# Performance work log

Measured on AMD Instinct MI355X. Metric: run time of the kernel, lower is better.

## Reference

```python
import jax, jax.numpy as jnp
import numpy as np

N, E, DIN, DH, DOUT = 50000, 800000, 256, 128, 64


def setup_inputs() -> dict:
    key = jax.random.key(0)
    ks = jax.random.split(key, 12)
    return {
        "h": jax.random.normal(ks[0], (N, DIN), jnp.float32),
        "src": jax.random.randint(ks[1], (E,), 0, N, jnp.int32),
        "dst": jax.random.randint(ks[2], (E,), 0, N, jnp.int32),
        "W1": jax.random.normal(ks[3], (DIN, DH), jnp.float32) * (DIN ** -0.5),
        "al1": jax.random.normal(ks[4], (DH,), jnp.float32) * (DH ** -0.5),
        "ar1": jax.random.normal(ks[5], (DH,), jnp.float32) * (DH ** -0.5),
        "W2": jax.random.normal(ks[6], (DH, DH), jnp.float32) * (DH ** -0.5),
        "al2": jax.random.normal(ks[7], (DH,), jnp.float32) * (DH ** -0.5),
        "ar2": jax.random.normal(ks[8], (DH,), jnp.float32) * (DH ** -0.5),
        "W3": jax.random.normal(ks[9], (DH, DOUT), jnp.float32) * (DH ** -0.5),
        "al3": jax.random.normal(ks[10], (DOUT,), jnp.float32) * (DOUT ** -0.5),
        "ar3": jax.random.normal(ks[11], (DOUT,), jnp.float32) * (DOUT ** -0.5),
    }


def gat_layer(h, W, al, ar, src, dst):
    """DGL GATConv, 1 head, no bias: proj -> leaky_relu edge scores -> edge softmax over dst -> scatter-sum."""
    n = h.shape[0]
    f = h @ W                                   # [N, d]
    el = f @ al                                 # [N]
    er = f @ ar                                 # [N]
    e = jax.nn.leaky_relu(el[src] + er[dst], negative_slope=0.2)  # [E]
    m = jax.ops.segment_max(e, dst, num_segments=n)
    m = jnp.where(jnp.isfinite(m), m, 0.0)      # zero-in-degree nodes
    m = jax.lax.stop_gradient(m)
    ex = jnp.exp(e - m[dst])                    # [E]
    z = jax.ops.segment_sum(ex, dst, num_segments=n)
    a = ex / jnp.maximum(z, 1e-9)[dst]          # [E] softmax weights
    return jax.ops.segment_sum(a[:, None] * f[src], dst, num_segments=n)


def reference(h, src, dst, W1, al1, ar1, W2, al2, ar2, W3, al3, ar3):
    x = gat_layer(h, W1, al1, ar1, src, dst)
    x = jax.nn.relu(x)                          # dropout = identity (eval)
    x = gat_layer(x, W2, al2, ar2, src, dst)
    x = jax.nn.relu(x)
    x = gat_layer(x, W3, al3, ar3, src, dst)    # mean over 1 head = identity
    return jax.nn.log_softmax(x, axis=-1)
```

## Files before the change

kernel.cpp:

```cpp
#include <hip/hip_runtime.h>
#include <math.h>

#define DIN 256
#define DHID 128
#define DOUTC 64
#define EPB 2048

typedef __attribute__((ext_vector_type(8))) short short8;
typedef __attribute__((ext_vector_type(4))) float f32x4;

static __device__ __forceinline__ float wave_max(float v){
  #pragma unroll
  for (int o=1;o<64;o<<=1) v = fmaxf(v, __shfl_xor(v,o,64));
  return v;
}
static __device__ __forceinline__ float wave_sum(float v){
  #pragma unroll
  for (int o=1;o<64;o<<=1) v += __shfl_xor(v,o,64);
  return v;
}

static __device__ __forceinline__ unsigned short bf16_rne(float x){
  unsigned int u = __float_as_uint(x);
  return (unsigned short)((u + 0x7FFFu + ((u>>16)&1u)) >> 16);
}
static __device__ __forceinline__ float bf16_to_f32(unsigned short h){
  return __uint_as_float(((unsigned int)h)<<16);
}
static __device__ __forceinline__ float blo(unsigned int u){ return __uint_as_float(u<<16); }
static __device__ __forceinline__ float bhi(unsigned int u){ return __uint_as_float(u & 0xffff0000u); }

__global__ __launch_bounds__(256) void rs_hist(const int* __restrict__ dst,
    int* __restrict__ ghist, int E, int NB){
  __shared__ int h[256];
  const int t = threadIdx.x, blk = blockIdx.x;
  h[t] = 0; __syncthreads();
  const int base = blk*EPB;
  #pragma unroll
  for (int i=0;i<EPB/256;i++){
    int j = base + i*256 + t;
    if (j < E) atomicAdd(&h[dst[j]>>8], 1);
  }
  __syncthreads();
  ghist[t*NB + blk] = h[t];
}

__global__ __launch_bounds__(256) void rs_scan(int* __restrict__ ghist,
    int* __restrict__ btot, int NB){
  __shared__ int b[256];
  __shared__ int carry;
  const int hb = blockIdx.x, t = threadIdx.x;
  if (t==0) carry = 0;
  __syncthreads();
  for (int c0=0; c0<NB; c0+=256){
    int i = c0 + t;
    int v = (i<NB)? ghist[hb*NB+i] : 0;
    b[t] = v; __syncthreads();
    #pragma unroll
    for (int o=1;o<256;o<<=1){
      int x = (t>=o)? b[t-o] : 0;
      __syncthreads();
      b[t] += x;
      __syncthreads();
    }
    if (i<NB) ghist[hb*NB+i] = carry + b[t] - v;
    __syncthreads();
    if (t==255) carry += b[255];
    __syncthreads();
  }
  if (t==255) btot[hb] = carry;
}

__global__ __launch_bounds__(256) void rs_scan2(int* __restrict__ btot,
    int* __restrict__ offsets, int N, int E){
  __shared__ int b[256];
  const int t = threadIdx.x;
  int v = btot[t];
  b[t] = v; __syncthreads();
  #pragma unroll
  for (int o=1;o<256;o<<=1){
    int x = (t>=o)? b[t-o] : 0;
    __syncthreads();
    b[t] += x;
    __syncthreads();
  }
  btot[t] = b[t] - v;
  if (t==255){ btot[256] = E; offsets[N] = E; }
}

__global__ __launch_bounds__(256) void rs_scatter(const int* __restrict__ src,
    const int* __restrict__ dst, const int* __restrict__ ghist,
    const int* __restrict__ btot, unsigned int* __restrict__ ebuf, int E, int NB){
  __shared__ int cur[256];
  const int t = threadIdx.x, blk = blockIdx.x;
  cur[t] = ghist[t*NB + blk] + btot[t];
  __syncthreads();
  const int base = blk*EPB;
  #pragma unroll
  for (int i=0;i<EPB/256;i++){
    int j = base + i*256 + t;
    if (j < E){
      int d = dst[j];
      int pos = atomicAdd(&cur[d>>8], 1);
      ebuf[pos] = ((unsigned)src[j] << 8) | ((unsigned)d & 255u);
    }
  }
}

__global__ __launch_bounds__(256) void bucket_sort(const unsigned int* __restrict__ ebuf,
    const int* __restrict__ btot, int* __restrict__ offsets,
    int* __restrict__ srcs, int N){
  __shared__ int h[256];
  __shared__ int b[256];
  const int hb = blockIdx.x, t = threadIdx.x;
  const int b0 = btot[hb], b1 = btot[hb+1];
  h[t] = 0; __syncthreads();
  for (int j=b0+t; j<b1; j+=256) atomicAdd(&h[ebuf[j] & 255u], 1);
  __syncthreads();
  int v = h[t];
  b[t] = v; __syncthreads();
  #pragma unroll
  for (int o=1;o<256;o<<=1){
    int x = (t>=o)? b[t-o] : 0;
    __syncthreads();
    b[t] += x;
    __syncthreads();
  }
  const int excl = b[t] - v;
  const int node = hb*256 + t;
  if (node < N) offsets[node] = b0 + excl;
  h[t] = excl;
  __syncthreads();
  for (int j=b0+t; j<b1; j+=256){
    unsigned int e = ebuf[j];
    int pos = b0 + atomicAdd(&h[e & 255u], 1);
    srcs[pos] = (int)(e >> 8);
  }
}

template<int K, int NC>
static __device__ __forceinline__ void pack_one(const float* __restrict__ W,
    unsigned short* __restrict__ Wp, int idx){
  constexpr int CT = NC/16;
  int l = idx & 63, t = idx >> 6;
  int ct = t % CT, kt = t / CT;
  int col = ct*16 + (l & 15);
  int k0 = kt*32 + (l >> 4)*8;
  unsigned short* dstp = Wp + (size_t)idx*8;
  #pragma unroll
  for (int j=0;j<8;j++)
    dstp[j] = bf16_rne(W[(size_t)(k0+j)*NC + col]);
}

__global__ __launch_bounds__(256) void pack_all(const float* __restrict__ W1,
    const float* __restrict__ W2, const float* __restrict__ W3,
    unsigned short* __restrict__ Wp1, unsigned short* __restrict__ Wp2,
    unsigned short* __restrict__ Wp3){
  constexpr int N1 = (DIN/32)*(DHID/16)*64;
  constexpr int N2 = (DHID/32)*(DHID/16)*64;
  constexpr int N3 = (DHID/32)*(DOUTC/16)*64;
  int idx = blockIdx.x*256 + threadIdx.x;
  if (idx < N1) pack_one<DIN,DHID>(W1, Wp1, idx);
  else if (idx < N1+N2) pack_one<DHID,DHID>(W2, Wp2, idx-N1);
  else if (idx < N1+N2+N3) pack_one<DHID,DOUTC>(W3, Wp3, idx-N1-N2);
}

template<int K, int NC>
__global__ __launch_bounds__(256) void gemm_v3(const float* __restrict__ A,
    const unsigned short* __restrict__ Wp,
    const float* __restrict__ al, const float* __restrict__ ar,
    unsigned short* __restrict__ Fb, float* __restrict__ el, float* __restrict__ er, int nrows)
{
  constexpr int CT = NC/16, KT = K/32;
  constexpr int CHUNK_KT = (32/CT) < KT ? (32/CT) : KT;
  constexpr int NCHUNK = KT / CHUNK_KT;
  constexpr int CHUNK_SHORTS = CHUNK_KT*CT*64*8;
  __shared__ unsigned short bsm[CHUNK_SHORTS];

  const int tid = threadIdx.x;
  const int lane = tid & 63;
  const int wid  = tid >> 6;
  const int row0 = blockIdx.x*64 + wid*16;
  const int c = lane & 15, g = lane >> 4;
  const int arow = row0 + c;
  const bool aok = arow < nrows;

  f32x4 acc[CT];
  #pragma unroll
  for (int i=0;i<CT;i++) acc[i] = (f32x4)0.f;

  for (int ch=0; ch<NCHUNK; ++ch){
    if (ch) __syncthreads();
    {
      const uint4* gsrc = (const uint4*)Wp + (size_t)ch*(CHUNK_SHORTS/8);
      uint4* ldst = (uint4*)bsm;
      #pragma unroll
      for (int i=0; i<CHUNK_SHORTS/8/256; ++i)
        ldst[i*256 + tid] = gsrc[i*256 + tid];
    }
    __syncthreads();

    #pragma unroll
    for (int ktl=0; ktl<CHUNK_KT; ++ktl){
      const int k0 = (ch*CHUNK_KT + ktl)*32 + g*8;
      float xs[8];
      if (aok){
        float4 v0 = *(const float4*)&A[(size_t)arow*K + k0];
        float4 v1 = *(const float4*)&A[(size_t)arow*K + k0 + 4];
        xs[0]=v0.x; xs[1]=v0.y; xs[2]=v0.z; xs[3]=v0.w;
        xs[4]=v1.x; xs[5]=v1.y; xs[6]=v1.z; xs[7]=v1.w;
      } else {
        #pragma unroll
        for (int j=0;j<8;j++) xs[j]=0.f;
      }
      short8 ahi, alo;
      #pragma unroll
      for (int j=0;j<8;j++){
        unsigned short hh = bf16_rne(xs[j]);
        ahi[j] = (short)hh;
        alo[j] = (short)bf16_rne(xs[j] - bf16_to_f32(hh));
      }
      #pragma unroll
      for (int ct=0; ct<CT; ++ct){
        short8 b = *(const short8*)&bsm[(ktl*CT+ct)*512 + lane*8];
        acc[ct] = __builtin_amdgcn_mfma_f32_16x16x32_bf16(ahi, b, acc[ct], 0,0,0);
        acc[ct] = __builtin_amdgcn_mfma_f32_16x16x32_bf16(alo, b, acc[ct], 0,0,0);
      }
    }
  }

  float alv[CT], arv[CT];
  #pragma unroll
  for (int ct=0;ct<CT;ct++){ alv[ct]=al[ct*16+c]; arv[ct]=ar[ct*16+c]; }
  #pragma unroll
  for (int j=0;j<4;j++){
    const int row = row0 + g*4 + j;
    const bool ok = row < nrows;
    float sl=0.f, sr=0.f;
    #pragma unroll
    for (int ct=0;ct<CT;ct++){
      float f = acc[ct][j];
      sl = fmaf(f, alv[ct], sl);
      sr = fmaf(f, arv[ct], sr);
      if (ok) Fb[(size_t)row*NC + ct*16 + c] = bf16_rne(f);
    }
    #pragma unroll
    for (int o=1;o<16;o<<=1){ sl += __shfl_xor(sl,o,64); sr += __shfl_xor(sr,o,64); }
    if (ok && c==0){ el[row]=sl; er[row]=sr; }
  }
}

template<int D, bool RELU, bool LOGSM>
__global__ __launch_bounds__(256) void agg7_kernel(const unsigned short* __restrict__ Fb,
    const float* __restrict__ el, const float* __restrict__ er,
    const int* __restrict__ offsets, const int* __restrict__ srcs,
    float* __restrict__ out, int N)
{
  constexpr int CPL = D/16;
  __shared__ float2 ws[4][64];
  const int wv = threadIdx.x >> 6;
  const int lane = threadIdx.x & 63;
  const int c16 = lane & 15, g = lane >> 4;
  const int v = blockIdx.x*4 + wv;
  if (v >= N) return;
  const int o0 = offsets[v], o1 = offsets[v+1];
  const float erv = er[v];

  float zlane = 0.f;
  float acc[CPL];
  #pragma unroll
  for (int i=0;i<CPL;i++) acc[i]=0.f;

  for (int s0 = o0; s0 < o1; s0 += 64){
    const int j = s0 + lane;
    int sidx = 0; float wgt = 0.f;
    if (j < o1){
      sidx = srcs[j];
      float tv = el[sidx] + erv;
      tv = (tv > 0.f) ? tv : 0.2f*tv;
      wgt = __expf(tv);
    }
    zlane += wgt;
    ws[wv][lane] = make_float2(wgt, __int_as_float(sidx));
    __builtin_amdgcn_wave_barrier();

    const int cnt = min(64, o1 - s0);
    int t = g;
    if constexpr (D == 128){
      for (; t+4 < cnt; t += 8){
        float2 p0 = ws[wv][t], p1 = ws[wv][t+4];
        uint4 u0 = *((const uint4*)(Fb + (size_t)__float_as_int(p0.y)*128) + c16);
        uint4 u1 = *((const uint4*)(Fb + (size_t)__float_as_int(p1.y)*128) + c16);
        acc[0]=fmaf(p0.x, blo(u0.x), acc[0]); acc[1]=fmaf(p0.x, bhi(u0.x), acc[1]);
        acc[2]=fmaf(p0.x, blo(u0.y), acc[2]); acc[3]=fmaf(p0.x, bhi(u0.y), acc[3]);
        acc[4]=fmaf(p0.x, blo(u0.z), acc[4]); acc[5]=fmaf(p0.x, bhi(u0.z), acc[5]);
        acc[6]=fmaf(p0.x, blo(u0.w), acc[6]); acc[7]=fmaf(p0.x, bhi(u0.w), acc[7]);
        acc[0]=fmaf(p1.x, blo(u1.x), acc[0]); acc[1]=fmaf(p1.x, bhi(u1.x), acc[1]);
        acc[2]=fmaf(p1.x, blo(u1.y), acc[2]); acc[3]=fmaf(p1.x, bhi(u1.y), acc[3]);
        acc[4]=fmaf(p1.x, blo(u1.z), acc[4]); acc[5]=fmaf(p1.x, bhi(u1.z), acc[5]);
        acc[6]=fmaf(p1.x, blo(u1.w), acc[6]); acc[7]=fmaf(p1.x, bhi(u1.w), acc[7]);
      }
      if (t < cnt){
        float2 p0 = ws[wv][t];
        uint4 u0 = *((const uint4*)(Fb + (size_t)__float_as_int(p0.y)*128) + c16);
        acc[0]=fmaf(p0.x, blo(u0.x), acc[0]); acc[1]=fmaf(p0.x, bhi(u0.x), acc[1]);
        acc[2]=fmaf(p0.x, blo(u0.y), acc[2]); acc[3]=fmaf(p0.x, bhi(u0.y), acc[3]);
        acc[4]=fmaf(p0.x, blo(u0.z), acc[4]); acc[5]=fmaf(p0.x, bhi(u0.z), acc[5]);
        acc[6]=fmaf(p0.x, blo(u0.w), acc[6]); acc[7]=fmaf(p0.x, bhi(u0.w), acc[7]);
      }
    } else {
      for (; t+4 < cnt; t += 8){
        float2 p0 = ws[wv][t], p1 = ws[wv][t+4];
        uint2 u0 = *((const uint2*)(Fb + (size_t)__float_as_int(p0.y)*64) + c16);
        uint2 u1 = *((const uint2*)(Fb + (size_t)__float_as_int(p1.y)*64) + c16);
        acc[0]=fmaf(p0.x, blo(u0.x), acc[0]); acc[1]=fmaf(p0.x, bhi(u0.x), acc[1]);
        acc[2]=fmaf(p0.x, blo(u0.y), acc[2]); acc[3]=fmaf(p0.x, bhi(u0.y), acc[3]);
        acc[0]=fmaf(p1.x, blo(u1.x), acc[0]); acc[1]=fmaf(p1.x, bhi(u1.x), acc[1]);
        acc[2]=fmaf(p1.x, blo(u1.y), acc[2]); acc[3]=fmaf(p1.x, bhi(u1.y), acc[3]);
      }
      if (t < cnt){
        float2 p0 = ws[wv][t];
        uint2 u0 = *((const uint2*)(Fb + (size_t)__float_as_int(p0.y)*64) + c16);
        acc[0]=fmaf(p0.x, blo(u0.x), acc[0]); acc[1]=fmaf(p0.x, bhi(u0.x), acc[1]);
        acc[2]=fmaf(p0.x, blo(u0.y), acc[2]); acc[3]=fmaf(p0.x, bhi(u0.y), acc[3]);
      }
    }
    __builtin_amdgcn_wave_barrier();
  }

  #pragma unroll
  for (int i=0;i<CPL;i++){
    acc[i] += __shfl_xor(acc[i],16,64);
    acc[i] += __shfl_xor(acc[i],32,64);
  }
  const float z = wave_sum(zlane);
  const float zi = 1.f / fmaxf(z, 1e-9f);

  if constexpr (LOGSM){
    float y[CPL];
    #pragma unroll
    for (int i=0;i<CPL;i++) y[i] = acc[i]*zi;
    float M = y[0];
    #pragma unroll
    for (int i=1;i<CPL;i++) M = fmaxf(M, y[i]);
    #pragma unroll
    for (int o=1;o<16;o<<=1) M = fmaxf(M, __shfl_xor(M,o,64));
    float ssum = 0.f;
    #pragma unroll
    for (int i=0;i<CPL;i++) ssum += __expf(y[i]-M);
    #pragma unroll
    for (int o=1;o<16;o<<=1) ssum += __shfl_xor(ssum,o,64);
    const float lw = M + logf(ssum);
    if (g==0){
      float4 r = make_float4(y[0]-lw, y[1]-lw, y[2]-lw, y[3]-lw);
      *(float4*)&out[(size_t)v*64 + c16*4] = r;
    }
  } else {
    if (g==0){
      float r[CPL];
      #pragma unroll
      for (int i=0;i<CPL;i++){ r[i]=acc[i]*zi; if (RELU) r[i]=fmaxf(r[i],0.f); }
      *(float4*)&out[(size_t)v*128 + c16*8]     = make_float4(r[0],r[1],r[2],r[3]);
      *(float4*)&out[(size_t)v*128 + c16*8 + 4] = make_float4(r[4],r[5],r[6],r[7]);
    }
  }
}

extern "C" void kernel_launch(void* const* d_in, const int* in_sizes, int n_in,
                              void* d_out, int out_size, void* d_ws, size_t ws_size,
                              hipStream_t stream) {
  const float* h   = (const float*)d_in[0];
  const int*   src = (const int*)d_in[1];
  const int*   dst = (const int*)d_in[2];
  const float* W1  = (const float*)d_in[3];
  const float* al1 = (const float*)d_in[4];
  const float* ar1 = (const float*)d_in[5];
  const float* W2  = (const float*)d_in[6];
  const float* al2 = (const float*)d_in[7];
  const float* ar2 = (const float*)d_in[8];
  const float* W3  = (const float*)d_in[9];
  const float* al3 = (const float*)d_in[10];
  const float* ar3 = (const float*)d_in[11];

  const int N = in_sizes[0] / DIN;
  const int E = in_sizes[1];
  const int NB = (E + EPB - 1) / EPB;
  const int NHB = (N + 255) / 256;

  auto alignup = [](size_t x){ return (x + 255) & ~(size_t)255; };
  char* p = (char*)d_ws;
  int* offsets = (int*)p; p += alignup(((size_t)N+1)*4);
  int* srcs    = (int*)p; p += alignup((size_t)E*4);
  int* ghist   = (int*)p; p += alignup((size_t)256*NB*4);
  int* btot    = (int*)p; p += alignup(257*4);
  unsigned int* ebuf = (unsigned int*)p; p += alignup((size_t)E*4);
  unsigned short* Fb = (unsigned short*)p; p += alignup((size_t)N*DHID*2);
  float* X     = (float*)p; p += alignup((size_t)N*DHID*4);
  float* el    = (float*)p; p += alignup((size_t)N*4);
  float* er    = (float*)p; p += alignup((size_t)N*4);
  unsigned short* Wp1 = (unsigned short*)p; p += alignup((size_t)(DIN/32)*(DHID/16)*64*8*2);
  unsigned short* Wp2 = (unsigned short*)p; p += alignup((size_t)(DHID/32)*(DHID/16)*64*8*2);
  unsigned short* Wp3 = (unsigned short*)p; p += alignup((size_t)(DHID/32)*(DOUTC/16)*64*8*2);

  const int nbW4 = (N+3)/4;
  const int nbG  = (N+63)/64;

  pack_all<<<28,256,0,stream>>>(W1, W2, W3, Wp1, Wp2, Wp3);

  rs_hist   <<<NB, 256,0,stream>>>(dst, ghist, E, NB);
  rs_scan   <<<256,256,0,stream>>>(ghist, btot, NB);
  rs_scan2  <<<1,  256,0,stream>>>(btot, offsets, N, E);
  rs_scatter<<<NB, 256,0,stream>>>(src, dst, ghist, btot, ebuf, E, NB);
  bucket_sort<<<NHB,256,0,stream>>>(ebuf, btot, offsets, srcs, N);

  gemm_v3<DIN,DHID><<<nbG,256,0,stream>>>(h, Wp1, al1, ar1, Fb, el, er, N);
  agg7_kernel<128,true,false><<<nbW4,256,0,stream>>>(Fb, el, er, offsets, srcs, X, N);

  gemm_v3<DHID,DHID><<<nbG,256,0,stream>>>(X, Wp2, al2, ar2, Fb, el, er, N);
  agg7_kernel<128,true,false><<<nbW4,256,0,stream>>>(Fb, el, er, offsets, srcs, X, N);

  gemm_v3<DHID,DOUTC><<<nbG,256,0,stream>>>(X, Wp3, al3, ar3, Fb, el, er, N);
  agg7_kernel<64,false,true><<<nbW4,256,0,stream>>>(Fb, el, er, offsets, srcs, (float*)d_out, N);
}
```

Measured before the change: 169.7 us.

## Fuse CSR build and weight packing into one cooperative kernel with grid syncs

Merges the six preprocessing kernels (weight pack, histogram, two scans, scatter, bucket sort) into a single cooperative launch, using grid-wide syncs between phases. Weight packing runs alongside the histogram on extra blocks. The aim is to remove per-launch gaps and tail effects for these small kernels. In exchange, grid syncs add their own cost, and the grid (about 391+28 blocks) must fit co-resident or the launch fails.

```diff
diff --git a/kernel.cpp b/kernel.cpp
--- a/kernel.cpp
+++ b/kernel.cpp
@@ -1,4 +1,5 @@
 #include <hip/hip_runtime.h>
+#include <hip/hip_cooperative_groups.h>
 #include <math.h>
 
 #define DIN 256
@@ -9,11 +10,6 @@
 typedef __attribute__((ext_vector_type(8))) short short8;
 typedef __attribute__((ext_vector_type(4))) float f32x4;
 
-static __device__ __forceinline__ float wave_max(float v){
-  #pragma unroll
-  for (int o=1;o<64;o<<=1) v = fmaxf(v, __shfl_xor(v,o,64));
-  return v;
-}
 static __device__ __forceinline__ float wave_sum(float v){
   #pragma unroll
   for (int o=1;o<64;o<<=1) v += __shfl_xor(v,o,64);
@@ -29,114 +25,6 @@
 }
 static __device__ __forceinline__ float blo(unsigned int u){ return __uint_as_float(u<<16); }
 static __device__ __forceinline__ float bhi(unsigned int u){ return __uint_as_float(u & 0xffff0000u); }
-
-__global__ __launch_bounds__(256) void rs_hist(const int* __restrict__ dst,
-    int* __restrict__ ghist, int E, int NB){
-  __shared__ int h[256];
-  const int t = threadIdx.x, blk = blockIdx.x;
-  h[t] = 0; __syncthreads();
-  const int base = blk*EPB;
-  #pragma unroll
-  for (int i=0;i<EPB/256;i++){
-    int j = base + i*256 + t;
-    if (j < E) atomicAdd(&h[dst[j]>>8], 1);
-  }
-  __syncthreads();
-  ghist[t*NB + blk] = h[t];
-}
-
-__global__ __launch_bounds__(256) void rs_scan(int* __restrict__ ghist,
-    int* __restrict__ btot, int NB){
-  __shared__ int b[256];
-  __shared__ int carry;
-  const int hb = blockIdx.x, t = threadIdx.x;
-  if (t==0) carry = 0;
-  __syncthreads();
-  for (int c0=0; c0<NB; c0+=256){
-    int i = c0 + t;
-    int v = (i<NB)? ghist[hb*NB+i] : 0;
-    b[t] = v; __syncthreads();
-    #pragma unroll
-    for (int o=1;o<256;o<<=1){
-      int x = (t>=o)? b[t-o] : 0;
-      __syncthreads();
-      b[t] += x;
-      __syncthreads();
-    }
-    if (i<NB) ghist[hb*NB+i] = carry + b[t] - v;
-    __syncthreads();
-    if (t==255) carry += b[255];
-    __syncthreads();
-  }
-  if (t==255) btot[hb] = carry;
-}
-
-__global__ __launch_bounds__(256) void rs_scan2(int* __restrict__ btot,
-    int* __restrict__ offsets, int N, int E){
-  __shared__ int b[256];
-  const int t = threadIdx.x;
-  int v = btot[t];
-  b[t] = v; __syncthreads();
-  #pragma unroll
-  for (int o=1;o<256;o<<=1){
-    int x = (t>=o)? b[t-o] : 0;
-    __syncthreads();
-    b[t] += x;
-    __syncthreads();
-  }
-  btot[t] = b[t] - v;
-  if (t==255){ btot[256] = E; offsets[N] = E; }
-}
-
-__global__ __launch_bounds__(256) void rs_scatter(const int* __restrict__ src,
-    const int* __restrict__ dst, const int* __restrict__ ghist,
-    const int* __restrict__ btot, unsigned int* __restrict__ ebuf, int E, int NB){
-  __shared__ int cur[256];
-  const int t = threadIdx.x, blk = blockIdx.x;
-  cur[t] = ghist[t*NB + blk] + btot[t];
-  __syncthreads();
-  const int base = blk*EPB;
-  #pragma unroll
-  for (int i=0;i<EPB/256;i++){
-    int j = base + i*256 + t;
-    if (j < E){
-      int d = dst[j];
-      int pos = atomicAdd(&cur[d>>8], 1);
-      ebuf[pos] = ((unsigned)src[j] << 8) | ((unsigned)d & 255u);
-    }
-  }
-}
-
-__global__ __launch_bounds__(256) void bucket_sort(const unsigned int* __restrict__ ebuf,
-    const int* __restrict__ btot, int* __restrict__ offsets,
-    int* __restrict__ srcs, int N){
-  __shared__ int h[256];
-  __shared__ int b[256];
-  const int hb = blockIdx.x, t = threadIdx.x;
-  const int b0 = btot[hb], b1 = btot[hb+1];
-  h[t] = 0; __syncthreads();
-  for (int j=b0+t; j<b1; j+=256) atomicAdd(&h[ebuf[j] & 255u], 1);
-  __syncthreads();
-  int v = h[t];
-  b[t] = v; __syncthreads();
-  #pragma unroll
-  for (int o=1;o<256;o<<=1){
-    int x = (t>=o)? b[t-o] : 0;
-    __syncthreads();
-    b[t] += x;
-    __syncthreads();
-  }
-  const int excl = b[t] - v;
-  const int node = hb*256 + t;
-  if (node < N) offsets[node] = b0 + excl;
-  h[t] = excl;
-  __syncthreads();
-  for (int j=b0+t; j<b1; j+=256){
-    unsigned int e = ebuf[j];
-    int pos = b0 + atomicAdd(&h[e & 255u], 1);
-    srcs[pos] = (int)(e >> 8);
-  }
-}
 
 template<int K, int NC>
 static __device__ __forceinline__ void pack_one(const float* __restrict__ W,
@@ -152,17 +40,118 @@
     dstp[j] = bf16_rne(W[(size_t)(k0+j)*NC + col]);
 }
 
-__global__ __launch_bounds__(256) void pack_all(const float* __restrict__ W1,
-    const float* __restrict__ W2, const float* __restrict__ W3,
-    unsigned short* __restrict__ Wp1, unsigned short* __restrict__ Wp2,
-    unsigned short* __restrict__ Wp3){
-  constexpr int N1 = (DIN/32)*(DHID/16)*64;
-  constexpr int N2 = (DHID/32)*(DHID/16)*64;
-  constexpr int N3 = (DHID/32)*(DOUTC/16)*64;
-  int idx = blockIdx.x*256 + threadIdx.x;
-  if (idx < N1) pack_one<DIN,DHID>(W1, Wp1, idx);
-  else if (idx < N1+N2) pack_one<DHID,DHID>(W2, Wp2, idx-N1);
-  else if (idx < N1+N2+N3) pack_one<DHID,DOUTC>(W3, Wp3, idx-N1-N2);
+__global__ __launch_bounds__(256) void csr_coop(
+    const int* __restrict__ src, const int* __restrict__ dst,
+    const float* __restrict__ W1, const float* __restrict__ W2, const float* __restrict__ W3,
+    unsigned short* __restrict__ Wp1, unsigned short* __restrict__ Wp2, unsigned short* __restrict__ Wp3,
+    int* __restrict__ ghist, int* __restrict__ btot, int* __restrict__ offsets,
+    unsigned int* __restrict__ ebuf, int* __restrict__ srcs,
+    int E, int N, int NB, int NHB)
+{
+  cooperative_groups::grid_group gg = cooperative_groups::this_grid();
+  __shared__ int h[256];
+  __shared__ int b[256];
+  const int t = threadIdx.x, blk = blockIdx.x;
+
+  if (blk < NB){
+    h[t] = 0; __syncthreads();
+    const int base = blk*EPB;
+    #pragma unroll
+    for (int i=0;i<EPB/256;i++){
+      int j = base + i*256 + t;
+      if (j < E) atomicAdd(&h[dst[j]>>8], 1);
+    }
+    __syncthreads();
+    ghist[t*NB + blk] = h[t];
+  } else {
+    int idx = (blk-NB)*256 + t;
+    constexpr int N1 = (DIN/32)*(DHID/16)*64;
+    constexpr int N2 = (DHID/32)*(DHID/16)*64;
+    constexpr int N3 = (DHID/32)*(DOUTC/16)*64;
+    if (idx < N1) pack_one<DIN,DHID>(W1, Wp1, idx);
+    else if (idx < N1+N2) pack_one<DHID,DHID>(W2, Wp2, idx-N1);
+    else if (idx < N1+N2+N3) pack_one<DHID,DOUTC>(W3, Wp3, idx-N1-N2);
+  }
+  gg.sync();
+
+  if (blk < 256){
+    int carry = 0;
+    for (int c0=0; c0<NB; c0+=256){
+      int i = c0 + t;
+      int v = (i<NB)? ghist[blk*NB+i] : 0;
+      b[t] = v; __syncthreads();
+      #pragma unroll
+      for (int o=1;o<256;o<<=1){
+        int x = (t>=o)? b[t-o] : 0;
+        __syncthreads();
+        b[t] += x;
+        __syncthreads();
+      }
+      if (i<NB) ghist[blk*NB+i] = carry + b[t] - v;
+      __syncthreads();
+      carry += b[255];
+      __syncthreads();
+    }
+    if (t==255) btot[blk] = carry;
+  }
+  gg.sync();
+
+  if (blk == 0){
+    int v = btot[t];
+    b[t] = v; __syncthreads();
+    #pragma unroll
+    for (int o=1;o<256;o<<=1){
+      int x = (t>=o)? b[t-o] : 0;
+      __syncthreads();
+      b[t] += x;
+      __syncthreads();
+    }
+    btot[t] = b[t] - v;
+    if (t==255){ btot[256] = E; offsets[N] = E; }
+  }
+  gg.sync();
+
+  if (blk < NB){
+    h[t] = ghist[t*NB + blk] + btot[t];
+    __syncthreads();
+    const int base = blk*EPB;
+    #pragma unroll
+    for (int i=0;i<EPB/256;i++){
+      int j = base + i*256 + t;
+      if (j < E){
+        int d = dst[j];
+        int pos = atomicAdd(&h[d>>8], 1);
+        ebuf[pos] = ((unsigned)src[j] << 8) | ((unsigned)d & 255u);
+      }
+    }
+  }
+  gg.sync();
+
+  if (blk < NHB){
+    const int b0 = btot[blk], b1 = btot[blk+1];
+    h[t] = 0; __syncthreads();
+    for (int j=b0+t; j<b1; j+=256) atomicAdd(&h[ebuf[j] & 255u], 1);
+    __syncthreads();
+    int v = h[t];
+    b[t] = v; __syncthreads();
+    #pragma unroll
+    for (int o=1;o<256;o<<=1){
+      int x = (t>=o)? b[t-o] : 0;
+      __syncthreads();
+      b[t] += x;
+      __syncthreads();
+    }
+    const int excl = b[t] - v;
+    const int node = blk*256 + t;
+    if (node < N) offsets[node] = b0 + excl;
+    h[t] = excl;
+    __syncthreads();
+    for (int j=b0+t; j<b1; j+=256){
+      unsigned int e = ebuf[j];
+      int pos = b0 + atomicAdd(&h[e & 255u], 1);
+      srcs[pos] = (int)(e >> 8);
+    }
+  }
 }
 
 template<int K, int NC>
@@ -222,9 +211,9 @@
       }
       #pragma unroll
       for (int ct=0; ct<CT; ++ct){
-        short8 b = *(const short8*)&bsm[(ktl*CT+ct)*512 + lane*8];
-        acc[ct] = __builtin_amdgcn_mfma_f32_16x16x32_bf16(ahi, b, acc[ct], 0,0,0);
-        acc[ct] = __builtin_amdgcn_mfma_f32_16x16x32_bf16(alo, b, acc[ct], 0,0,0);
+        short8 bb = *(const short8*)&bsm[(ktl*CT+ct)*512 + lane*8];
+        acc[ct] = __builtin_amdgcn_mfma_f32_16x16x32_bf16(ahi, bb, acc[ct], 0,0,0);
+        acc[ct] = __builtin_amdgcn_mfma_f32_16x16x32_bf16(alo, bb, acc[ct], 0,0,0);
       }
     }
   }
@@ -405,13 +394,21 @@
   const int nbW4 = (N+3)/4;
   const int nbG  = (N+63)/64;
 
-  pack_all<<<28,256,0,stream>>>(W1, W2, W3, Wp1, Wp2, Wp3);
-
-  rs_hist   <<<NB, 256,0,stream>>>(dst, ghist, E, NB);
-  rs_scan   <<<256,256,0,stream>>>(ghist, btot, NB);
-  rs_scan2  <<<1,  256,0,stream>>>(btot, offsets, N, E);
-  rs_scatter<<<NB, 256,0,stream>>>(src, dst, ghist, btot, ebuf, E, NB);
-  bucket_sort<<<NHB,256,0,stream>>>(ebuf, btot, offsets, srcs, N);
+  int GB = NB + 28;
+  if (GB < 256) GB = 256;
+  if (GB < NHB) GB = NHB;
+  {
+    void* kargs[] = {
+      (void*)&src, (void*)&dst,
+      (void*)&W1, (void*)&W2, (void*)&W3,
+      (void*)&Wp1, (void*)&Wp2, (void*)&Wp3,
+      (void*)&ghist, (void*)&btot, (void*)&offsets,
+      (void*)&ebuf, (void*)&srcs,
+      (void*)&E, (void*)&N, (void*)&NB, (void*)&NHB
+    };
+    hipLaunchCooperativeKernel((const void*)csr_coop, dim3(GB), dim3(256),
+                               kargs, 0, stream);
+  }
 
   gemm_v3<DIN,DHID><<<nbG,256,0,stream>>>(h, Wp1, al1, ar1, Fb, el, er, N);
   agg7_kernel<128,true,false><<<nbW4,256,0,stream>>>(Fb, el, er, offsets, srcs, X, N);
```

Measured after the change: 379.3 us. +123.6%, slower.
